# Kernel optimization log

Hardware: AMD Instinct MI355X
Metric: run time of the kernel (lower is better)

## Reference

```python
import jax, jax.numpy as jnp
import numpy as np
import math

EPS = 1e-06
H = 16


def favorplus_features(x, proj, eps=EPS):
    # x: [B,h,T,dk], proj: [h,m,dk] -> [B,h,T,m]
    xw = jnp.einsum('bhtd,hmd->bhtm', x, proj)
    xw = xw - jnp.max(xw, axis=-1, keepdims=True)
    exp_part = jnp.exp(xw)
    x_norm_sq = jnp.sum(x * x, axis=-1, keepdims=True)
    base = jnp.exp(-0.5 * x_norm_sq)
    return exp_part * base + eps


def setup_inputs() -> dict:
    key = jax.random.key(0)
    ks = jax.random.split(key, 7)
    B, T, d = 4, 4096, 1024
    h, m = H, 256
    dk = d // h
    s = 1.0 / math.sqrt(d)  # keep activations O(1) so exp(-0.5||q||^2) is meaningful
    return {
        'x': jax.random.normal(ks[0], (B, T, d), jnp.float32),
        'Wq': jax.random.normal(ks[1], (d, d), jnp.float32) * s,
        'Wk': jax.random.normal(ks[2], (d, d), jnp.float32) * s,
        'Wv': jax.random.normal(ks[3], (d, d), jnp.float32) * s,
        'Wo': jax.random.normal(ks[4], (d, d), jnp.float32) * s,
        'bo': jnp.zeros((d,), jnp.float32),
        'proj': jax.random.normal(ks[5], (h, m, dk), jnp.float32),
    }


def reference(x, Wq, Wk, Wv, Wo, bo, proj):
    B, T, d = x.shape
    h = H
    dk = d // h
    m = proj.shape[1]

    def heads(W):
        # torch Linear: x @ W.T ; split heads -> [B,h,T,dk]
        return (x @ W.T).reshape(B, T, h, dk).transpose(0, 2, 1, 3)

    Q, K, V = heads(Wq), heads(Wk), heads(Wv)
    scale = 1.0 / math.sqrt(dk)
    phiQ = favorplus_features(Q * scale, proj) / math.sqrt(m)  # [B,h,T,m]
    phiK = favorplus_features(K * scale, proj) / math.sqrt(m)

    KV = jnp.einsum('bhtm,bhtd->bhmd', phiK, V)          # [B,h,m,dk]
    Ksum = jnp.sum(phiK, axis=2)                          # [B,h,m]
    num = jnp.einsum('bhtm,bhmd->bhtd', phiQ, KV)         # [B,h,T,dk]
    den = jnp.einsum('bhtm,bhm->bht', phiQ, Ksum)[..., None] + EPS
    out_heads = num / den                                  # [B,h,T,dk]
    merged = out_heads.transpose(0, 2, 1, 3).reshape(B, T, h * dk)
    return merged @ Wo.T + bo
```

## Files before the change

### kernel.cpp

```cpp
#include <hip/hip_runtime.h>

typedef unsigned short u16;
typedef __attribute__((ext_vector_type(8))) short s8v;
typedef __attribute__((ext_vector_type(4))) float f4v;
typedef __attribute__((ext_vector_type(8))) unsigned short u16x8;
typedef __attribute__((ext_vector_type(4))) unsigned short u16x4;

__device__ __forceinline__ float b2f(u16 u) {
  unsigned int v = ((unsigned int)u) << 16;
  float f;
  __builtin_memcpy(&f, &v, 4);
  return f;
}
__device__ __forceinline__ u16 f2b(float f) {
  unsigned int v;
  __builtin_memcpy(&v, &f, 4);
  v = v + 0x7fffu + ((v >> 16) & 1u);
  return (u16)(v >> 16);
}
__device__ __forceinline__ void gl_lds16(const void* g, void* l) {
  __builtin_amdgcn_global_load_lds((__attribute__((address_space(1))) void*)g,
                                   (__attribute__((address_space(3))) void*)l,
                                   16, 0, 0);
}
__device__ __forceinline__ f4v mfma16(s8v a, s8v b, f4v c) {
  return __builtin_amdgcn_mfma_f32_16x16x32_bf16(a, b, c, 0, 0, 0);
}

__global__ __launch_bounds__(256) void k_convert(
    const float* __restrict__ x, const float* __restrict__ wq,
    const float* __restrict__ wk, const float* __restrict__ wv,
    const float* __restrict__ wo, const float* __restrict__ proj,
    u16* __restrict__ xb, u16* __restrict__ wqb, u16* __restrict__ wkb,
    u16* __restrict__ wvb, u16* __restrict__ wob, u16* __restrict__ projb) {
  const int NX = 4194304, NW = 262144, NP = 65536;
  const int total = NX + 4 * NW + NP;
  for (int i = blockIdx.x * 256 + threadIdx.x; i < total; i += gridDim.x * 256) {
    const float* src;
    u16* dst;
    int off;
    float scale = 1.0f;
    if (i < NX) { src = x; dst = xb; off = i; }
    else if (i < NX + NW) { src = wq; dst = wqb; off = i - NX; }
    else if (i < NX + 2 * NW) { src = wk; dst = wkb; off = i - NX - NW; }
    else if (i < NX + 3 * NW) { src = wv; dst = wvb; off = i - NX - 2 * NW; }
    else if (i < NX + 4 * NW) { src = wo; dst = wob; off = i - NX - 3 * NW; }
    else { src = proj; dst = projb; off = i - NX - 4 * NW; scale = 0.125f; }
    const float4 v = reinterpret_cast<const float4*>(src)[off];
    u16x4 o;
    o[0] = f2b(v.x * scale); o[1] = f2b(v.y * scale);
    o[2] = f2b(v.z * scale); o[3] = f2b(v.w * scale);
    reinterpret_cast<u16x4*>(dst)[off] = o;
  }
}

template <int COUTF32, int NCB>
__global__ __launch_bounds__(256) void k_gemm_swz(
    const u16* __restrict__ A, const u16* __restrict__ W,
    void* __restrict__ Cq, void* __restrict__ Ck, void* __restrict__ Cv,
    const float* __restrict__ bias) {
  const int bid = blockIdx.x;
  const int xcd = bid & 7, slot = bid >> 3;
  const int yg = slot / NCB, cb = slot - yg * NCB;
  const long row0 = (long)(yg * 8 + xcd) * 128;
  const int wrow0 = cb * 128;
  void* C = (cb < 8) ? Cq : (cb < 16) ? Ck : Cv;
  const int col0 = (cb & 7) * 128;
  __shared__ u16 As[128 * 64];
  __shared__ u16 Bs[128 * 64];
  const int tid = threadIdx.x, w = tid >> 6, l = tid & 63;
  const int wr = w >> 1, wc = w & 1, fr = l & 15, fq = l >> 4;
  f4v acc[4][4];
#pragma unroll
  for (int i = 0; i < 4; ++i)
#pragma unroll
    for (int j = 0; j < 4; ++j) acc[i][j] = 0.f;
  const int lr = l >> 3, lc = l & 7;
  for (int kt = 0; kt < 16; ++kt) {
    const int k0 = kt << 6;
    __syncthreads();
#pragma unroll
    for (int q = 0; q < 4; ++q) {
      const int r = q * 32 + w * 8 + lr;
      const int sc = (lc ^ (r & 7)) << 3;
      gl_lds16(A + (row0 + r) * 1024L + k0 + sc, (char*)As + q * 4096 + w * 1024);
      gl_lds16(W + (wrow0 + r) * 1024L + k0 + sc, (char*)Bs + q * 4096 + w * 1024);
    }
    __syncthreads();
#pragma unroll
    for (int ks = 0; ks < 2; ++ks) {
      s8v af[4], bf[4];
#pragma unroll
      for (int i = 0; i < 4; ++i) {
        const int R = wr * 64 + i * 16 + fr;
        af[i] = *(const s8v*)&As[R * 64 + (((ks * 4 + fq) ^ (R & 7)) << 3)];
      }
#pragma unroll
      for (int j = 0; j < 4; ++j) {
        const int R = wc * 64 + j * 16 + fr;
        bf[j] = *(const s8v*)&Bs[R * 64 + (((ks * 4 + fq) ^ (R & 7)) << 3)];
      }
#pragma unroll
      for (int i = 0; i < 4; ++i)
#pragma unroll
        for (int j = 0; j < 4; ++j) acc[i][j] = mfma16(af[i], bf[j], acc[i][j]);
    }
  }
  if (COUTF32) {
#pragma unroll
    for (int j = 0; j < 4; ++j) {
      const int col = col0 + wc * 64 + j * 16 + fr;
      const float bv = bias ? bias[col] : 0.f;
#pragma unroll
      for (int i = 0; i < 4; ++i) {
        const long row = row0 + wr * 64 + i * 16 + fq * 4;
#pragma unroll
        for (int r = 0; r < 4; ++r)
          ((float*)C)[(row + r) * 1024L + col] = acc[i][j][r] + bv;
      }
    }
  } else {
    __syncthreads();
    u16* myl = As + w * 1024;
    const int rr2 = l >> 2, c2 = (l & 3) * 16;
#pragma unroll
    for (int i = 0; i < 4; ++i) {
#pragma unroll
      for (int j = 0; j < 4; ++j)
#pragma unroll
        for (int r = 0; r < 4; ++r)
          myl[(fq * 4 + r) * 64 + j * 16 + fr] = f2b(acc[i][j][r]);
      const u16x8 o0 = *(const u16x8*)&myl[rr2 * 64 + c2];
      const u16x8 o1 = *(const u16x8*)&myl[rr2 * 64 + c2 + 8];
      u16* dst = (u16*)C + (row0 + wr * 64 + i * 16 + rr2) * 1024L + col0 + wc * 64 + c2;
      *(u16x8*)dst = o0;
      *(u16x8*)(dst + 8) = o1;
    }
  }
}

__global__ __launch_bounds__(512) void k_kvfused(
    const u16* __restrict__ Kb, const u16* __restrict__ Vb,
    const u16* __restrict__ projb, float* __restrict__ kvp,
    float* __restrict__ ksp) {
  __shared__ u16 Ps[256 * 72];
  __shared__ u16 PhiT[256 * 136];
  __shared__ u16 Ks[128 * 72];
  __shared__ u16 VT[64 * 136];
  __shared__ float norms[128];
  const int tid = threadIdx.x, w = tid >> 6, l = tid & 63;
  const int fr = l & 15, fq = l >> 4;
  const int c = blockIdx.x, bh = blockIdx.y, b = bh >> 4, h = bh & 15;
#pragma unroll
  for (int q = 0; q < 4; ++q) {
    const int flat = q * 4096 + tid * 8;
    const int m = flat >> 6, cc = flat & 63;
    *(u16x8*)&Ps[m * 72 + cc] = *(const u16x8*)&projb[h * 16384 + flat];
  }
  f4v kacc[2][4];
  float ksum = 0.f;
#pragma unroll
  for (int i = 0; i < 2; ++i)
#pragma unroll
    for (int j = 0; j < 4; ++j) kacc[i][j] = 0.f;
  for (int it = 0; it < 8; ++it) {
    const long t0 = (long)c * 1024 + it * 128;
    __syncthreads();
#pragma unroll
    for (int q = 0; q < 2; ++q) {
      const int flat = q * 4096 + tid * 8;
      const int r = flat >> 6, cc = flat & 63;
      *(u16x8*)&Ks[r * 72 + cc] =
          *(const u16x8*)&Kb[((long)b * 4096 + t0 + r) * 1024 + h * 64 + cc];
    }
    const long vrow = ((long)b * 4096 + t0 + (tid >> 2)) * 1024 + h * 64 + (tid & 3) * 16;
    const u16x8 v0 = *(const u16x8*)&Vb[vrow];
    const u16x8 v1 = *(const u16x8*)&Vb[vrow + 8];
    __syncthreads();
    {
      const int row = tid >> 2, part = tid & 3;
      const u16x8 a0 = *(const u16x8*)&Ks[row * 72 + part * 16];
      const u16x8 a1 = *(const u16x8*)&Ks[row * 72 + part * 16 + 8];
      float s = 0.f;
#pragma unroll
      for (int jj = 0; jj < 8; ++jj) { const float v = b2f(a0[jj]); s += v * v; }
#pragma unroll
      for (int jj = 0; jj < 8; ++jj) { const float v = b2f(a1[jj]); s += v * v; }
      s += __shfl_xor(s, 1);
      s += __shfl_xor(s, 2);
      if (part == 0) norms[row] = s * 0.015625f;
    }
    f4v pacc[16];
#pragma unroll
    for (int f = 0; f < 16; ++f) pacc[f] = 0.f;
#pragma unroll
    for (int ks = 0; ks < 2; ++ks) {
      const s8v a = *(const s8v*)&Ks[(w * 16 + fr) * 72 + ks * 32 + fq * 8];
#pragma unroll
      for (int f = 0; f < 16; ++f) {
        const s8v bb = *(const s8v*)&Ps[(f * 16 + fr) * 72 + ks * 32 + fq * 8];
        pacc[f] = mfma16(a, bb, pacc[f]);
      }
    }
    __syncthreads();
    float mx[4] = {-3.4e38f, -3.4e38f, -3.4e38f, -3.4e38f};
#pragma unroll
    for (int f = 0; f < 16; ++f)
#pragma unroll
      for (int r = 0; r < 4; ++r) mx[r] = fmaxf(mx[r], pacc[f][r]);
#pragma unroll
    for (int sft = 1; sft < 16; sft <<= 1)
#pragma unroll
      for (int r = 0; r < 4; ++r) mx[r] = fmaxf(mx[r], __shfl_xor(mx[r], sft));
    float nsq[4];
#pragma unroll
    for (int r = 0; r < 4; ++r) nsq[r] = norms[w * 16 + fq * 4 + r];
#pragma unroll
    for (int f = 0; f < 16; ++f) {
      u16x4 o;
#pragma unroll
      for (int r = 0; r < 4; ++r)
        o[r] = f2b((__expf(pacc[f][r] - mx[r] - 0.5f * nsq[r]) + 1e-6f) * 0.0625f);
      *(u16x4*)&PhiT[(f * 16 + fr) * 136 + w * 16 + fq * 4] = o;
    }
    {
      const int t = tid >> 2, e0 = (tid & 3) * 16;
#pragma unroll
      for (int jj = 0; jj < 8; ++jj) VT[(e0 + jj) * 136 + t] = v0[jj];
#pragma unroll
      for (int jj = 0; jj < 8; ++jj) VT[(e0 + 8 + jj) * 136 + t] = v1[jj];
    }
    __syncthreads();
#pragma unroll
    for (int ks = 0; ks < 4; ++ks) {
      s8v af[2], bf[4];
#pragma unroll
      for (int i = 0; i < 2; ++i)
        af[i] = *(const s8v*)&PhiT[(w * 32 + i * 16 + fr) * 136 + ks * 32 + fq * 8];
#pragma unroll
      for (int j = 0; j < 4; ++j)
        bf[j] = *(const s8v*)&VT[(j * 16 + fr) * 136 + ks * 32 + fq * 8];
#pragma unroll
      for (int i = 0; i < 2; ++i)
#pragma unroll
        for (int j = 0; j < 4; ++j) kacc[i][j] = mfma16(af[i], bf[j], kacc[i][j]);
    }
    if (tid < 256) {
#pragma unroll
      for (int t8 = 0; t8 < 16; ++t8) {
        const u16x8 p = *(const u16x8*)&PhiT[tid * 136 + t8 * 8];
#pragma unroll
        for (int jj = 0; jj < 8; ++jj) ksum += b2f(p[jj]);
      }
    }
  }
  const long obase = (long)(c * 64 + bh) * 16384;
#pragma unroll
  for (int i = 0; i < 2; ++i) {
    const int m = w * 32 + i * 16 + fq * 4;
#pragma unroll
    for (int j = 0; j < 4; ++j)
#pragma unroll
      for (int r = 0; r < 4; ++r)
        kvp[obase + (long)(m + r) * 64 + j * 16 + fr] = kacc[i][j][r];
  }
  if (tid < 256) ksp[(long)(c * 64 + bh) * 256 + tid] = ksum;
}

__global__ __launch_bounds__(256) void k_red(
    const float* __restrict__ kvp, const float* __restrict__ ksp,
    u16* __restrict__ KVT, float* __restrict__ ksumf) {
  const int bh = blockIdx.x, qq = blockIdx.y, tid = threadIdx.x;
  for (int it = 0; it < 16; ++it) {
    const int idx = (qq * 16 + it) * 256 + tid;
    const int m = idx >> 6, e = idx & 63;
    float s = 0.f;
#pragma unroll
    for (int cc = 0; cc < 4; ++cc)
      s += kvp[(long)(cc * 64 + bh) * 16384 + (long)m * 64 + e];
    KVT[(long)bh * 16384 + (long)e * 256 + m] = f2b(s);
  }
  if (qq == 0) {
    float s = 0.f;
#pragma unroll
    for (int cc = 0; cc < 4; ++cc) s += ksp[(long)(cc * 64 + bh) * 256 + tid];
    ksumf[bh * 256 + tid] = s;
  }
}

__global__ __launch_bounds__(512) void k_numfused(
    const u16* __restrict__ Qb, const u16* __restrict__ projb,
    const u16* __restrict__ KVT, const float* __restrict__ ksumf,
    u16* __restrict__ merged) {
  __shared__ u16 Ps[256 * 72];
  __shared__ u16 Qs[128 * 72];
  __shared__ u16 Phi[128 * 264];
  __shared__ u16 Bs[64 * 264];
  __shared__ float ksl[256];
  __shared__ float denA[128];
  __shared__ float norms[128];
  const int tid = threadIdx.x, w = tid >> 6, l = tid & 63;
  const int fr = l & 15, fq = l >> 4;
  const int tt = blockIdx.x, bh = blockIdx.y, b = bh >> 4, h = bh & 15;
#pragma unroll
  for (int q = 0; q < 4; ++q) {
    const int flat = q * 4096 + tid * 8;
    const int m = flat >> 6, cc = flat & 63;
    *(u16x8*)&Ps[m * 72 + cc] = *(const u16x8*)&projb[h * 16384 + flat];
  }
#pragma unroll
  for (int q = 0; q < 2; ++q) {
    const int flat = q * 4096 + tid * 8;
    const int r = flat >> 6, cc = flat & 63;
    *(u16x8*)&Qs[r * 72 + cc] =
        *(const u16x8*)&Qb[((long)b * 4096 + tt * 128 + r) * 1024 + h * 64 + cc];
  }
  {
    const int e = tid >> 3, seg = (tid & 7) * 32;
#pragma unroll
    for (int k = 0; k < 4; ++k) {
      const u16x8 vv = *(const u16x8*)&KVT[(long)bh * 16384 + e * 256 + seg + k * 8];
      *(u16x8*)&Bs[e * 264 + seg + k * 8] = vv;
    }
  }
  if (tid < 256) ksl[tid] = ksumf[bh * 256 + tid];
  __syncthreads();
  {
    const int row = tid >> 2, part = tid & 3;
    const u16x8 a0 = *(const u16x8*)&Qs[row * 72 + part * 16];
    const u16x8 a1 = *(const u16x8*)&Qs[row * 72 + part * 16 + 8];
    float s = 0.f;
#pragma unroll
    for (int jj = 0; jj < 8; ++jj) { const float v = b2f(a0[jj]); s += v * v; }
#pragma unroll
    for (int jj = 0; jj < 8; ++jj) { const float v = b2f(a1[jj]); s += v * v; }
    s += __shfl_xor(s, 1);
    s += __shfl_xor(s, 2);
    if (part == 0) norms[row] = s * 0.015625f;
  }
  f4v pacc[16];
#pragma unroll
  for (int f = 0; f < 16; ++f) pacc[f] = 0.f;
#pragma unroll
  for (int ks = 0; ks < 2; ++ks) {
    const s8v a = *(const s8v*)&Qs[(w * 16 + fr) * 72 + ks * 32 + fq * 8];
#pragma unroll
    for (int f = 0; f < 16; ++f) {
      const s8v bb = *(const s8v*)&Ps[(f * 16 + fr) * 72 + ks * 32 + fq * 8];
      pacc[f] = mfma16(a, bb, pacc[f]);
    }
  }
  __syncthreads();
  float mx[4] = {-3.4e38f, -3.4e38f, -3.4e38f, -3.4e38f};
#pragma unroll
  for (int f = 0; f < 16; ++f)
#pragma unroll
    for (int r = 0; r < 4; ++r) mx[r] = fmaxf(mx[r], pacc[f][r]);
#pragma unroll
  for (int sft = 1; sft < 16; sft <<= 1)
#pragma unroll
    for (int r = 0; r < 4; ++r) mx[r] = fmaxf(mx[r], __shfl_xor(mx[r], sft));
  float nsq[4];
#pragma unroll
  for (int r = 0; r < 4; ++r) nsq[r] = norms[w * 16 + fq * 4 + r];
#pragma unroll
  for (int f = 0; f < 16; ++f)
#pragma unroll
    for (int r = 0; r < 4; ++r)
      Phi[(w * 16 + fq * 4 + r) * 264 + f * 16 + fr] =
          f2b((__expf(pacc[f][r] - mx[r] - 0.5f * nsq[r]) + 1e-6f) * 0.0625f);
  __syncthreads();
  {
    const int row = tid >> 2, part = tid & 3;
    float d = 0.f;
#pragma unroll
    for (int j8 = 0; j8 < 8; ++j8) {
      const u16x8 p = *(const u16x8*)&Phi[row * 264 + part * 64 + j8 * 8];
      const float4 k0 = *(const float4*)&ksl[part * 64 + j8 * 8];
      const float4 k1 = *(const float4*)&ksl[part * 64 + j8 * 8 + 4];
      d += b2f(p[0]) * k0.x; d += b2f(p[1]) * k0.y;
      d += b2f(p[2]) * k0.z; d += b2f(p[3]) * k0.w;
      d += b2f(p[4]) * k1.x; d += b2f(p[5]) * k1.y;
      d += b2f(p[6]) * k1.z; d += b2f(p[7]) * k1.w;
    }
    d += __shfl_xor(d, 1);
    d += __shfl_xor(d, 2);
    if (part == 0) denA[row] = d;
  }
  f4v acc[4];
#pragma unroll
  for (int j = 0; j < 4; ++j) acc[j] = 0.f;
#pragma unroll
  for (int kt = 0; kt < 8; ++kt) {
    const s8v af = *(const s8v*)&Phi[(w * 16 + fr) * 264 + kt * 32 + fq * 8];
#pragma unroll
    for (int j = 0; j < 4; ++j) {
      const s8v bb = *(const s8v*)&Bs[(j * 16 + fr) * 264 + kt * 32 + fq * 8];
      acc[j] = mfma16(af, bb, acc[j]);
    }
  }
  __syncthreads();
#pragma unroll
  for (int r = 0; r < 4; ++r) {
    const float rd = 1.0f / (denA[w * 16 + fq * 4 + r] + 1e-6f);
    const long t = (long)tt * 128 + w * 16 + fq * 4 + r;
    const long gb = ((long)b * 4096 + t) * 1024 + h * 64;
#pragma unroll
    for (int j = 0; j < 4; ++j)
      merged[gb + j * 16 + fr] = f2b(acc[j][r] * rd);
  }
}

extern "C" void kernel_launch(void* const* d_in, const int* in_sizes, int n_in,
                              void* d_out, int out_size, void* d_ws, size_t ws_size,
                              hipStream_t stream) {
  const float* x = (const float*)d_in[0];
  const float* Wq = (const float*)d_in[1];
  const float* Wk = (const float*)d_in[2];
  const float* Wv = (const float*)d_in[3];
  const float* Wo = (const float*)d_in[4];
  const float* bo = (const float*)d_in[5];
  const float* proj = (const float*)d_in[6];
  char* ws = (char*)d_ws;
  u16* Vout = (u16*)d_out;
  u16* xb = (u16*)(ws + 0L);
  u16* wqb = (u16*)(ws + 33554432L);
  u16* wkb = (u16*)(ws + 35651584L);
  u16* wvb = (u16*)(ws + 37748736L);
  u16* wob = (u16*)(ws + 39845888L);
  u16* projb = (u16*)(ws + 41943040L);
  u16* Qb = (u16*)(ws + 42467328L);
  u16* Kb = (u16*)(ws + 76021760L);
  u16* KVT = (u16*)(ws + 109576192L);
  float* ksumf = (float*)(ws + 111673344L);
  float* kvp = (float*)xb;
  float* ksp = (float*)(ws + 16777216L);
  u16* merged = Kb;
  (void)in_sizes; (void)n_in; (void)out_size; (void)ws_size;

  k_convert<<<dim3(2048), dim3(256), 0, stream>>>(x, Wq, Wk, Wv, Wo, proj,
                                                  xb, wqb, wkb, wvb, wob, projb);
  k_gemm_swz<0, 24><<<dim3(3072), dim3(256), 0, stream>>>(
      xb, wqb, Qb, Kb, Vout, nullptr);
  k_kvfused<<<dim3(4, 64), dim3(512), 0, stream>>>(Kb, Vout, projb, kvp, ksp);
  k_red<<<dim3(64, 4), dim3(256), 0, stream>>>(kvp, ksp, KVT, ksumf);
  k_numfused<<<dim3(32, 64), dim3(512), 0, stream>>>(Qb, projb, KVT, ksumf, merged);
  k_gemm_swz<1, 8><<<dim3(1024), dim3(256), 0, stream>>>(
      merged, wob, d_out, d_out, d_out, bo);
}
```

Measured before the change: 336.5 us.

## Prefetch K/V tiles in registers; read proj/KVT directly from global in numfused

In the KV-accumulation kernel, the next iteration's K and V tiles are loaded into registers while the current tile is computed, and the V transpose into LDS moves to the top of the loop. This aims to overlap global load latency with compute. In k_numfused, the proj and KVT staging buffers in LDS are removed: MFMA B fragments are read straight from global/L2, and Qs aliases the Phi buffer. The smaller LDS footprint plus launch_bounds(512,4) targets higher occupancy, at the cost of uncached global fragment reads and more register pressure.

New measurement: 392.9 us. +16.8%, slower.

```diff
diff --git a/kernel.cpp b/kernel.cpp
--- a/kernel.cpp
+++ b/kernel.cpp
@@ -163,20 +163,29 @@
   for (int i = 0; i < 2; ++i)
 #pragma unroll
     for (int j = 0; j < 4; ++j) kacc[i][j] = 0.f;
+  const int kr = tid >> 3, kc = (tid & 7) * 8;
+  const int vt = tid >> 2, ve0 = (tid & 3) * 16;
+  const long kbase = (long)b * 4096 + (long)c * 1024;
+  u16x8 ck0 = *(const u16x8*)&Kb[(kbase + kr) * 1024 + h * 64 + kc];
+  u16x8 ck1 = *(const u16x8*)&Kb[(kbase + 64 + kr) * 1024 + h * 64 + kc];
+  u16x8 cv0 = *(const u16x8*)&Vb[(kbase + vt) * 1024 + h * 64 + ve0];
+  u16x8 cv1 = *(const u16x8*)&Vb[(kbase + vt) * 1024 + h * 64 + ve0 + 8];
   for (int it = 0; it < 8; ++it) {
-    const long t0 = (long)c * 1024 + it * 128;
-    __syncthreads();
-#pragma unroll
-    for (int q = 0; q < 2; ++q) {
-      const int flat = q * 4096 + tid * 8;
-      const int r = flat >> 6, cc = flat & 63;
-      *(u16x8*)&Ks[r * 72 + cc] =
-          *(const u16x8*)&Kb[((long)b * 4096 + t0 + r) * 1024 + h * 64 + cc];
-    }
-    const long vrow = ((long)b * 4096 + t0 + (tid >> 2)) * 1024 + h * 64 + (tid & 3) * 16;
-    const u16x8 v0 = *(const u16x8*)&Vb[vrow];
-    const u16x8 v1 = *(const u16x8*)&Vb[vrow + 8];
-    __syncthreads();
+    __syncthreads();
+    *(u16x8*)&Ks[kr * 72 + kc] = ck0;
+    *(u16x8*)&Ks[(64 + kr) * 72 + kc] = ck1;
+#pragma unroll
+    for (int jj = 0; jj < 8; ++jj) VT[(ve0 + jj) * 136 + vt] = cv0[jj];
+#pragma unroll
+    for (int jj = 0; jj < 8; ++jj) VT[(ve0 + 8 + jj) * 136 + vt] = cv1[jj];
+    __syncthreads();
+    if (it < 7) {
+      const long t0n = kbase + (it + 1) * 128;
+      ck0 = *(const u16x8*)&Kb[(t0n + kr) * 1024 + h * 64 + kc];
+      ck1 = *(const u16x8*)&Kb[(t0n + 64 + kr) * 1024 + h * 64 + kc];
+      cv0 = *(const u16x8*)&Vb[(t0n + vt) * 1024 + h * 64 + ve0];
+      cv1 = *(const u16x8*)&Vb[(t0n + vt) * 1024 + h * 64 + ve0 + 8];
+    }
     {
       const int row = tid >> 2, part = tid & 3;
       const u16x8 a0 = *(const u16x8*)&Ks[row * 72 + part * 16];
@@ -222,13 +231,6 @@
       for (int r = 0; r < 4; ++r)
         o[r] = f2b((__expf(pacc[f][r] - mx[r] - 0.5f * nsq[r]) + 1e-6f) * 0.0625f);
       *(u16x4*)&PhiT[(f * 16 + fr) * 136 + w * 16 + fq * 4] = o;
-    }
-    {
-      const int t = tid >> 2, e0 = (tid & 3) * 16;
-#pragma unroll
-      for (int jj = 0; jj < 8; ++jj) VT[(e0 + jj) * 136 + t] = v0[jj];
-#pragma unroll
-      for (int jj = 0; jj < 8; ++jj) VT[(e0 + 8 + jj) * 136 + t] = v1[jj];
     }
     __syncthreads();
 #pragma unroll
@@ -288,40 +290,27 @@
   }
 }
 
-__global__ __launch_bounds__(512) void k_numfused(
+__global__ __launch_bounds__(512, 4) void k_numfused(
     const u16* __restrict__ Qb, const u16* __restrict__ projb,
     const u16* __restrict__ KVT, const float* __restrict__ ksumf,
     u16* __restrict__ merged) {
-  __shared__ u16 Ps[256 * 72];
-  __shared__ u16 Qs[128 * 72];
-  __shared__ u16 Phi[128 * 264];
-  __shared__ u16 Bs[64 * 264];
+  __shared__ __align__(16) char UN[128 * 264 * 2];
+  u16* Qs = (u16*)UN;
+  u16* Phi = (u16*)UN;
   __shared__ float ksl[256];
   __shared__ float denA[128];
   __shared__ float norms[128];
   const int tid = threadIdx.x, w = tid >> 6, l = tid & 63;
   const int fr = l & 15, fq = l >> 4;
   const int tt = blockIdx.x, bh = blockIdx.y, b = bh >> 4, h = bh & 15;
-#pragma unroll
-  for (int q = 0; q < 4; ++q) {
-    const int flat = q * 4096 + tid * 8;
-    const int m = flat >> 6, cc = flat & 63;
-    *(u16x8*)&Ps[m * 72 + cc] = *(const u16x8*)&projb[h * 16384 + flat];
-  }
+  const u16* projH = projb + h * 16384;
+  const u16* kvtH = KVT + (long)bh * 16384;
 #pragma unroll
   for (int q = 0; q < 2; ++q) {
     const int flat = q * 4096 + tid * 8;
     const int r = flat >> 6, cc = flat & 63;
     *(u16x8*)&Qs[r * 72 + cc] =
         *(const u16x8*)&Qb[((long)b * 4096 + tt * 128 + r) * 1024 + h * 64 + cc];
-  }
-  {
-    const int e = tid >> 3, seg = (tid & 7) * 32;
-#pragma unroll
-    for (int k = 0; k < 4; ++k) {
-      const u16x8 vv = *(const u16x8*)&KVT[(long)bh * 16384 + e * 256 + seg + k * 8];
-      *(u16x8*)&Bs[e * 264 + seg + k * 8] = vv;
-    }
   }
   if (tid < 256) ksl[tid] = ksumf[bh * 256 + tid];
   __syncthreads();
@@ -346,7 +335,7 @@
     const s8v a = *(const s8v*)&Qs[(w * 16 + fr) * 72 + ks * 32 + fq * 8];
 #pragma unroll
     for (int f = 0; f < 16; ++f) {
-      const s8v bb = *(const s8v*)&Ps[(f * 16 + fr) * 72 + ks * 32 + fq * 8];
+      const s8v bb = *(const s8v*)&projH[(f * 16 + fr) * 64 + ks * 32 + fq * 8];
       pacc[f] = mfma16(a, bb, pacc[f]);
     }
   }
@@ -395,7 +384,7 @@
     const s8v af = *(const s8v*)&Phi[(w * 16 + fr) * 264 + kt * 32 + fq * 8];
 #pragma unroll
     for (int j = 0; j < 4; ++j) {
-      const s8v bb = *(const s8v*)&Bs[(j * 16 + fr) * 264 + kt * 32 + fq * 8];
+      const s8v bb = *(const s8v*)&kvtH[(j * 16 + fr) * 256 + kt * 32 + fq * 8];
       acc[j] = mfma16(af, bb, acc[j]);
     }
   }
```
